# Performance work log

Measured on AMD Instinct MI355X. Metric: run time of the kernel, lower is better.

## Reference

```python
import jax, jax.numpy as jnp
import numpy as np

EPS = 1e-9
ALPHA = 1.0
BETA = 6.0
TOPK = 13
NUM_CLASSES = 80


def _make_boxes(key, shape, img=640.0, wh_min=8.0, wh_max=128.0):
    k1, k2 = jax.random.split(key)
    cxy = jax.random.uniform(k1, shape[:-1] + (2,)) * img
    wh = wh_min + jax.random.uniform(k2, shape[:-1] + (2,)) * (wh_max - wh_min)
    return jnp.concatenate([cxy - wh / 2, cxy + wh / 2], axis=-1)


def setup_inputs() -> dict:
    key = jax.random.key(0)
    ks = jax.random.split(key, 5)
    B, N, C, M = 16, 8400, NUM_CLASSES, 64
    pd_scores = jax.random.normal(ks[0], (B, N, C), dtype=jnp.float32)  # logits
    pd_bboxes = _make_boxes(ks[1], (B, N, 4))
    anc_points = jax.random.uniform(ks[2], (N, 2)) * 640.0
    gt_labels = jax.random.randint(ks[3], (B, M, 1), 0, C).astype(jnp.int64)
    gt_bboxes = _make_boxes(ks[4], (B, M, 4), wh_min=16.0, wh_max=256.0)
    mask_gt = jnp.ones((B, M, 1), dtype=jnp.float32)
    return {"pd_scores": pd_scores, "pd_bboxes": pd_bboxes, "anc_points": anc_points,
            "gt_labels": gt_labels, "gt_bboxes": gt_bboxes, "mask_gt": mask_gt}


def _pairwise_iou(gt_bboxes, pd_bboxes):
    # gt: (B,M,4), pd: (B,N,4) -> (B,M,N)
    a1 = gt_bboxes[:, :, None, :2]
    a2 = gt_bboxes[:, :, None, 2:]
    b1 = pd_bboxes[:, None, :, :2]
    b2 = pd_bboxes[:, None, :, 2:]
    inter = jnp.clip(jnp.minimum(a2, b2) - jnp.maximum(a1, b1), 0.0).prod(-1)
    area_a = (a2 - a1).prod(-1)
    area_b = (b2 - b1).prod(-1)
    return inter / jnp.maximum(area_a + area_b - inter, EPS)


def _tal_assign(pd_scores, pd_bboxes, anc_points, gt_labels, gt_bboxes, mask_gt):
    B, N, C = pd_scores.shape
    M = gt_labels.shape[1]
    ps = jax.nn.sigmoid(pd_scores)  # input_is_logits=True
    mask_gt_bool = mask_gt[..., 0] > 0.5  # (B,M)

    # centers-in-boxes mask (B,M,N)
    xy = anc_points[None, None, :, :]
    lt = gt_bboxes[:, :, None, :2]
    rb = gt_bboxes[:, :, None, 2:]
    deltas = jnp.concatenate([xy - lt, rb - xy], axis=-1)  # (B,M,N,4)
    mask_in_gts = deltas.min(-1) > EPS
    valid = mask_in_gts & mask_gt_bool[:, :, None]

    # alignment metric: score(gt class)^alpha * IoU^beta, zero outside valid
    gt_ids = jnp.clip(gt_labels[..., 0], 0)  # (B,M)
    scores_t = jnp.swapaxes(ps, 1, 2)  # (B,C,N)
    bbox_scores = jnp.take_along_axis(scores_t, gt_ids[:, :, None], axis=1)  # (B,M,N)
    ious = _pairwise_iou(gt_bboxes, pd_bboxes)
    ious = jnp.where(valid, ious, 0.0)
    align = jnp.where(valid, (bbox_scores ** ALPHA) * (ious ** BETA), 0.0)

    # top-k anchors per GT along anchor dim
    topv, topi = jax.lax.top_k(align, TOPK)  # (B,M,K)
    sel = (topv > EPS) & mask_gt_bool[:, :, None]
    bi = jnp.arange(B)[:, None, None]
    mi = jnp.arange(M)[None, :, None]
    cnt = jnp.zeros((B, M, N), jnp.int32).at[bi, mi, topi].add(sel.astype(jnp.int32))
    topk_mask = cnt > 0
    mask_pos = (topk_mask & valid).astype(jnp.float32)  # (B,M,N)

    # resolve anchors assigned to multiple GTs: keep highest IoU GT
    fg = mask_pos.sum(axis=1)  # (B,N)
    multi = (fg > 1)[:, None, :]  # (B,1,N)
    best_gt = jnp.argmax(ious, axis=1)  # (B,N)
    is_max = jnp.swapaxes(jax.nn.one_hot(best_gt, M, dtype=mask_pos.dtype), 1, 2)  # (B,M,N)
    mask_pos = jnp.where(multi, is_max, mask_pos)
    fg_mask = mask_pos.sum(axis=1)  # (B,N)
    tgt_gt_idx = jnp.argmax(mask_pos, axis=1)  # (B,N)

    # gather targets
    target_labels = jnp.take_along_axis(gt_labels[..., 0], tgt_gt_idx, axis=1)  # (B,N)
    target_bboxes = jnp.take_along_axis(gt_bboxes, tgt_gt_idx[..., None], axis=1)  # (B,N,4)

    # normalized classification targets
    align = align * mask_pos
    max_align = align.max(axis=1, keepdims=True) + EPS  # (B,1,N)
    per_anchor = (align / max_align * (ious * mask_pos)).sum(axis=1)  # (B,N)
    onehot = jax.nn.one_hot(target_labels, C, dtype=jnp.float32)
    cls_targets = onehot * per_anchor[..., None]  # (B,N,C)
    return target_labels, target_bboxes, cls_targets, fg_mask > 0, tgt_gt_idx


def reference(pd_scores, pd_bboxes, anc_points, gt_labels, gt_bboxes, mask_gt):
    return _tal_assign(pd_scores, pd_bboxes, anc_points, gt_labels, gt_bboxes, mask_gt)
```

## Files before the change

kernel.cpp:

```cpp
#include <hip/hip_runtime.h>
#include <math.h>

#define BB 16
#define NN 8400
#define CC 80
#define MM 64
#define KTOP 13
#define FEPS 1e-9f
#define CAP 2048
#define RPW 8

typedef float floatx4 __attribute__((ext_vector_type(4)));
typedef unsigned long long u64;

#define OFF_O1 134400
#define OFF_O2 672000
#define OFF_O3 11424000
#define OFF_O4 11558400
#define CCNT_OFF 6153472
#define CAND_OFF 6154496
#define SCR_OFF  10348800

__device__ __forceinline__ float iou_pair(const float4 g, const float4 p) {
    float ix1 = fmaxf(g.x, p.x);
    float iy1 = fmaxf(g.y, p.y);
    float ix2 = fminf(g.z, p.z);
    float iy2 = fminf(g.w, p.w);
    float iw = fmaxf(ix2 - ix1, 0.0f);
    float ih = fmaxf(iy2 - iy1, 0.0f);
    float inter = iw * ih;
    float aa = (g.z - g.x) * (g.w - g.y);
    float ab = (p.z - p.x) * (p.w - p.y);
    float uni = fmaxf(aa + ab - inter, FEPS);
    return inter / uni;
}

__global__ __launch_bounds__(256) void k_zero2(int* __restrict__ ccnt,
                                               int* __restrict__ scr)
{
    int i = blockIdx.x * 256 + threadIdx.x;
    if (i < 1024) ccnt[i] = 0;
    else if (i < 1024 + 403200) scr[i - 1024] = 0;
}

__global__ __launch_bounds__(256) void k_align_emit(
    const float* __restrict__ pd_scores, const float* __restrict__ pd_bboxes,
    const float* __restrict__ anc, const int* __restrict__ gt_labels,
    const float* __restrict__ gt_bboxes, const float* __restrict__ mask_gt,
    int* __restrict__ ccnt, u64* __restrict__ cand)
{
    const int b = blockIdx.y;
    const int n = blockIdx.x * 256 + threadIdx.x;
    const int tid = threadIdx.x;

    __shared__ float4 gtb[MM];
    __shared__ int labS[MM];
    __shared__ int hcnt[MM];
    __shared__ int gbase[MM];

    if (tid < MM) {
        float4 g = *(const float4*)&gt_bboxes[(size_t)(b * MM + tid) * 4];
        if (mask_gt[b * MM + tid] <= 0.5f)
            g = make_float4(1e30f, 1e30f, -1e30f, -1e30f);
        gtb[tid] = g;
        int lb = gt_labels[b * MM + tid];
        labS[tid] = lb > 0 ? lb : 0;
        hcnt[tid] = 0;
    }
    __syncthreads();

    float ax = 0.0f, ay = 0.0f;
    const bool inb = n < NN;
    if (inb) { float2 a2 = *(const float2*)&anc[2 * n]; ax = a2.x; ay = a2.y; }

    u64 mask = 0ull;
    #pragma unroll 8
    for (int m = 0; m < MM; ++m) {
        float4 g = gtb[m];
        float d1 = ax - g.x, d2 = ay - g.y, d3 = g.z - ax, d4 = g.w - ay;
        if (inb && fminf(fminf(d1, d2), fminf(d3, d4)) > FEPS)
            mask |= 1ull << m;
    }

    u64 t = mask;
    while (t) { int m = __ffsll(t) - 1; t &= t - 1; atomicAdd(&hcnt[m], 1); }
    __syncthreads();
    if (tid < MM && hcnt[tid] > 0) {
        gbase[tid] = atomicAdd(&ccnt[b * MM + tid], hcnt[tid]);
        hcnt[tid] = 0;
    }
    __syncthreads();

    if (mask) {
        const float4 p = *(const float4*)&pd_bboxes[((size_t)b * NN + n) * 4];
        const float* srow = pd_scores + ((size_t)b * NN + n) * CC;
        t = mask;
        while (t) {
            int m = __ffsll(t) - 1; t &= t - 1;
            float io = iou_pair(gtb[m], p);
            int lab = labS[m];
            float4 c = *(const float4*)(srow + (lab & ~3));
            int r = lab & 3;
            float x = (r == 0) ? c.x : (r == 1) ? c.y : (r == 2) ? c.z : c.w;
            float s = 1.0f / (1.0f + expf(-x));
            float i2 = io * io;
            unsigned key = __float_as_uint(s * (i2 * i2 * i2));
            int slot = gbase[m] + atomicAdd(&hcnt[m], 1);
            if (slot < CAP)
                cand[(size_t)(b * MM + m) * CAP + slot] =
                    ((u64)key << 32) | (unsigned)(NN - n);
        }
    }
}

__global__ __launch_bounds__(256) void k_topk(
    const int* __restrict__ ccnt, const u64* __restrict__ cand,
    int* __restrict__ cntb, int* __restrict__ mselb, float* __restrict__ aselb)
{
    const int bm = blockIdx.x;
    const int b = bm >> 6, m = bm & 63;
    const int tid = threadIdx.x;
    const int lane = tid & 63;
    const int wid = tid >> 6;

    __shared__ u64 cmerge[64];

    const unsigned epskey = __float_as_uint(FEPS);
    const int count = min(ccnt[bm], CAP);
    const u64* list = cand + (size_t)bm * CAP;

    u64 e[RPW];
    #pragma unroll
    for (int j = 0; j < RPW; ++j) {
        int i = tid + j * 256;
        e[j] = (i < count) ? list[i] : 0ull;
    }

    {
        u64 lm = 0ull;
        #pragma unroll
        for (int j = 0; j < RPW; ++j) if (e[j] > lm) lm = e[j];

        u64 winv = 0ull;
        for (int r = 0; r < KTOP; ++r) {
            u64 bv = lm;
            #pragma unroll
            for (int off = 32; off > 0; off >>= 1) {
                u64 ov = __shfl_xor(bv, off, 64);
                if (ov > bv) bv = ov;
            }
            if ((unsigned)(bv >> 32) <= epskey) break;
            if (lane == r) winv = bv;
            if (lm == bv) {
                #pragma unroll
                for (int j = 0; j < RPW; ++j) if (e[j] == bv) e[j] = 0ull;
                lm = 0ull;
                #pragma unroll
                for (int j = 0; j < RPW; ++j) if (e[j] > lm) lm = e[j];
            }
        }
        if (lane < KTOP) cmerge[wid * KTOP + lane] = winv;
        if (wid == 0 && lane >= 4 * KTOP) cmerge[lane] = 0ull;
    }
    __syncthreads();

    if (wid == 0) {
        u64 v = cmerge[lane];
        u64 winv = 0ull;
        for (int r = 0; r < KTOP; ++r) {
            u64 bv = v;
            #pragma unroll
            for (int off = 32; off > 0; off >>= 1) {
                u64 ov = __shfl_xor(bv, off, 64);
                if (ov > bv) bv = ov;
            }
            if ((unsigned)(bv >> 32) <= epskey) break;
            if (lane == r) winv = bv;
            if (v == bv) v = 0ull;
        }
        if (lane < KTOP) {
            unsigned hk = (unsigned)(winv >> 32);
            if (hk > epskey) {
                int n = NN - (int)(winv & 0xFFFFFFFFull);
                int ai = b * NN + n;
                atomicAdd(&cntb[ai], 1);
                atomicAdd(&mselb[ai], m);
                atomicAdd(&aselb[ai], __uint_as_float(hk));
            }
        }
    }
}

__global__ __launch_bounds__(256) void k_assign(
    const float* __restrict__ pd_scores, const float* __restrict__ pd_bboxes,
    const float* __restrict__ anc, const int* __restrict__ gt_labels,
    const float* __restrict__ gt_bboxes, const float* __restrict__ mask_gt,
    const int* __restrict__ cntb, const int* __restrict__ mselb,
    const float* __restrict__ aselb,
    float* __restrict__ out0, float* __restrict__ out1,
    float* __restrict__ out3, float* __restrict__ out4,
    float* __restrict__ perb)
{
    const int b = blockIdx.y;
    const int n = blockIdx.x * 256 + threadIdx.x;

    __shared__ float4 gtb[MM];
    __shared__ int    labS[MM];
    __shared__ float  mgS[MM];
    if (threadIdx.x < MM) {
        int m = threadIdx.x;
        gtb[m]  = *(const float4*)&gt_bboxes[(size_t)(b * MM + m) * 4];
        labS[m] = gt_labels[b * MM + m];
        mgS[m]  = mask_gt[b * MM + m];
    }
    __syncthreads();
    if (n >= NN) return;

    const size_t idx = (size_t)b * NN + n;
    const int cnt = cntb[idx];

    float per = 0.0f, fg = 0.0f;
    int mstar = 0;

    if (cnt > 0) {
        fg = 1.0f;
        const float4 p = *(const float4*)&pd_bboxes[idx * 4];
        if (cnt == 1) {
            mstar = mselb[idx];
            float a = aselb[idx];
            float io = iou_pair(gtb[mstar], p);
            per = a / (a + FEPS) * io;
        } else {
            float2 a2 = *(const float2*)&anc[2 * n];
            float bestI = -1.0f; int bestM = 0;
            for (int m = 0; m < MM; ++m) {
                float4 gg = gtb[m];
                float d1 = a2.x - gg.x, d2 = a2.y - gg.y;
                float d3 = gg.z - a2.x, d4 = gg.w - a2.y;
                bool valid = (fminf(fminf(d1, d2), fminf(d3, d4)) > FEPS) &&
                             (mgS[m] > 0.5f);
                float io = valid ? iou_pair(gg, p) : 0.0f;
                if (io > bestI) { bestI = io; bestM = m; }
            }
            mstar = bestM;
            float io = bestI;
            int lb = labS[mstar]; int lbc = lb > 0 ? lb : 0;
            float x = pd_scores[idx * CC + lbc];
            float s = 1.0f / (1.0f + expf(-x));
            float i2 = io * io;
            float a = s * (i2 * i2 * i2);
            per = a / (a + FEPS) * io;
        }
    }

    out0[idx] = (float)labS[mstar];
    ((float4*)out1)[idx] = gtb[mstar];
    out3[idx] = fg;
    out4[idx] = (float)mstar;
    perb[idx] = per;
}

__global__ __launch_bounds__(256) void k_cls(
    const float* __restrict__ out0, const float* __restrict__ perb,
    floatx4* __restrict__ cls4)
{
    int i = blockIdx.x * 256 + threadIdx.x;
    if (i >= BB * NN * CC / 4) return;
    int row = i / 20;
    int c4 = (i - row * 20) * 4;
    int lab = (int)out0[row];
    float per = perb[row];
    int d = lab - c4;
    floatx4 v;
    v.x = (d == 0) ? per : 0.0f;
    v.y = (d == 1) ? per : 0.0f;
    v.z = (d == 2) ? per : 0.0f;
    v.w = (d == 3) ? per : 0.0f;
    __builtin_nontemporal_store(v, &cls4[i]);
}

extern "C" void kernel_launch(void* const* d_in, const int* in_sizes, int n_in,
                              void* d_out, int out_size, void* d_ws, size_t ws_size,
                              hipStream_t stream) {
    const float* pd_scores = (const float*)d_in[0];
    const float* pd_bboxes = (const float*)d_in[1];
    const float* anc       = (const float*)d_in[2];
    const int*   gt_labels = (const int*)d_in[3];
    const float* gt_bboxes = (const float*)d_in[4];
    const float* mask_gt   = (const float*)d_in[5];

    float* out  = (float*)d_out;
    float* out0 = out;
    float* out1 = out + OFF_O1;
    float* out2 = out + OFF_O2;
    float* out3 = out + OFF_O3;
    float* out4 = out + OFF_O4;

    int*   ccnt  = (int*)(out2 + CCNT_OFF);
    u64*   cand  = (u64*)(out2 + CAND_OFF);
    float* scr   = out2 + SCR_OFF;
    int*   cntb  = (int*)scr;
    int*   mselb = (int*)(scr + 134400);
    float* aselb = scr + 268800;
    float* perb  = (float*)d_ws;

    k_zero2<<<dim3((1024 + 403200 + 255) / 256), dim3(256), 0, stream>>>(
        ccnt, (int*)scr);

    k_align_emit<<<dim3((NN + 255) / 256, BB), dim3(256), 0, stream>>>(
        pd_scores, pd_bboxes, anc, gt_labels, gt_bboxes, mask_gt, ccnt, cand);

    k_topk<<<dim3(BB * MM), dim3(256), 0, stream>>>(
        ccnt, cand, cntb, mselb, aselb);

    k_assign<<<dim3((NN + 255) / 256, BB), dim3(256), 0, stream>>>(
        pd_scores, pd_bboxes, anc, gt_labels, gt_bboxes, mask_gt,
        cntb, mselb, aselb, out0, out1, out3, out4, perb);

    const int n4 = (BB * NN * CC) / 4;
    k_cls<<<dim3((n4 + 255) / 256), dim3(256), 0, stream>>>(out0, perb, (floatx4*)out2);
}
```

Before: 64.15 us.

## Fuse assign with cls write, stage score rows in LDS, move scratch to workspace

The class-target write kernel is folded into the assign kernel, so each block writes its own one-hot rows from per-anchor label and score values kept in shared memory. This removes one launch and the perb round trip. The emit kernel now stages contiguous score rows and predicted boxes through shared memory in coalesced chunks, and spreads each anchor's GT candidates across 8 lanes instead of one thread doing scattered gathers. Scratch buffers move from the cls output region into the workspace, which keeps them from colliding with the fused cls writes. In exchange, the emit kernel reads every score row and adds extra barriers.

```diff
diff --git a/kernel.cpp b/kernel.cpp
--- a/kernel.cpp
+++ b/kernel.cpp
@@ -17,9 +17,8 @@
 #define OFF_O2 672000
 #define OFF_O3 11424000
 #define OFF_O4 11558400
-#define CCNT_OFF 6153472
-#define CAND_OFF 6154496
-#define SCR_OFF  10348800
+
+#define ZERO_N (1024 + 3 * 134400)
 
 __device__ __forceinline__ float iou_pair(const float4 g, const float4 p) {
     float ix1 = fmaxf(g.x, p.x);
@@ -35,12 +34,10 @@
     return inter / uni;
 }
 
-__global__ __launch_bounds__(256) void k_zero2(int* __restrict__ ccnt,
-                                               int* __restrict__ scr)
+__global__ __launch_bounds__(256) void k_zero(int* __restrict__ p)
 {
     int i = blockIdx.x * 256 + threadIdx.x;
-    if (i < 1024) ccnt[i] = 0;
-    else if (i < 1024 + 403200) scr[i - 1024] = 0;
+    if (i < ZERO_N) p[i] = 0;
 }
 
 __global__ __launch_bounds__(256) void k_align_emit(
@@ -50,13 +47,17 @@
     int* __restrict__ ccnt, u64* __restrict__ cand)
 {
     const int b = blockIdx.y;
-    const int n = blockIdx.x * 256 + threadIdx.x;
     const int tid = threadIdx.x;
+    const int n0 = blockIdx.x * 256;
+    const int n = n0 + tid;
 
     __shared__ float4 gtb[MM];
-    __shared__ int labS[MM];
-    __shared__ int hcnt[MM];
-    __shared__ int gbase[MM];
+    __shared__ int    labS[MM];
+    __shared__ int    hcnt[MM];
+    __shared__ int    gbase[MM];
+    __shared__ u64    maskS[256];
+    __shared__ float4 srows4[640];
+    __shared__ float4 pbbS[32];
 
     if (tid < MM) {
         float4 g = *(const float4*)&gt_bboxes[(size_t)(b * MM + tid) * 4];
@@ -81,6 +82,7 @@
         if (inb && fminf(fminf(d1, d2), fminf(d3, d4)) > FEPS)
             mask |= 1ull << m;
     }
+    maskS[tid] = mask;
 
     u64 t = mask;
     while (t) { int m = __ffsll(t) - 1; t &= t - 1; atomicAdd(&hcnt[m], 1); }
@@ -89,26 +91,48 @@
         gbase[tid] = atomicAdd(&ccnt[b * MM + tid], hcnt[tid]);
         hcnt[tid] = 0;
     }
-    __syncthreads();
-
-    if (mask) {
-        const float4 p = *(const float4*)&pd_bboxes[((size_t)b * NN + n) * 4];
-        const float* srow = pd_scores + ((size_t)b * NN + n) * CC;
-        t = mask;
-        while (t) {
-            int m = __ffsll(t) - 1; t &= t - 1;
-            float io = iou_pair(gtb[m], p);
-            int lab = labS[m];
-            float4 c = *(const float4*)(srow + (lab & ~3));
-            int r = lab & 3;
-            float x = (r == 0) ? c.x : (r == 1) ? c.y : (r == 2) ? c.z : c.w;
-            float s = 1.0f / (1.0f + expf(-x));
-            float i2 = io * io;
-            unsigned key = __float_as_uint(s * (i2 * i2 * i2));
-            int slot = gbase[m] + atomicAdd(&hcnt[m], 1);
-            if (slot < CAP)
-                cand[(size_t)(b * MM + m) * CAP + slot] =
-                    ((u64)key << 32) | (unsigned)(NN - n);
+
+    const float4* src4 = (const float4*)(pd_scores + (size_t)b * NN * CC);
+    for (int sub = 0; sub < 8; ++sub) {
+        const int la0 = sub * 32;
+        const int gn0 = n0 + la0;
+        __syncthreads();
+        {
+            const int base4 = gn0 * 20;
+            #pragma unroll
+            for (int k = tid; k < 640; k += 256) {
+                int gf = base4 + k;
+                srows4[k] = (gf < NN * 20) ? src4[gf]
+                                           : make_float4(0.f, 0.f, 0.f, 0.f);
+            }
+            if (tid < 32) {
+                int gn = gn0 + tid;
+                pbbS[tid] = (gn < NN)
+                    ? *(const float4*)&pd_bboxes[((size_t)b * NN + gn) * 4]
+                    : make_float4(0.f, 0.f, 0.f, 0.f);
+            }
+        }
+        __syncthreads();
+
+        const int la = la0 + (tid >> 3);
+        const int r = tid & 7;
+        u64 tt = maskS[la] & (0x0101010101010101ull << r);
+        if (tt) {
+            const float4 p = pbbS[la - la0];
+            const float* row = (const float*)srows4 + (la - la0) * 80;
+            const int gn = n0 + la;
+            while (tt) {
+                int m = __ffsll(tt) - 1; tt &= tt - 1;
+                float io = iou_pair(gtb[m], p);
+                float x = row[labS[m]];
+                float s = 1.0f / (1.0f + expf(-x));
+                float i2 = io * io;
+                unsigned key = __float_as_uint(s * (i2 * i2 * i2));
+                int slot = gbase[m] + atomicAdd(&hcnt[m], 1);
+                if (slot < CAP)
+                    cand[(size_t)(b * MM + m) * CAP + slot] =
+                        ((u64)key << 32) | (unsigned)(NN - gn);
+            }
         }
     }
 }
@@ -191,7 +215,7 @@
     }
 }
 
-__global__ __launch_bounds__(256) void k_assign(
+__global__ __launch_bounds__(256) void k_assign_cls(
     const float* __restrict__ pd_scores, const float* __restrict__ pd_bboxes,
     const float* __restrict__ anc, const int* __restrict__ gt_labels,
     const float* __restrict__ gt_bboxes, const float* __restrict__ mask_gt,
@@ -199,84 +223,88 @@
     const float* __restrict__ aselb,
     float* __restrict__ out0, float* __restrict__ out1,
     float* __restrict__ out3, float* __restrict__ out4,
-    float* __restrict__ perb)
+    floatx4* __restrict__ cls4)
 {
     const int b = blockIdx.y;
-    const int n = blockIdx.x * 256 + threadIdx.x;
+    const int n0 = blockIdx.x * 256;
+    const int tid = threadIdx.x;
+    const int n = n0 + tid;
 
     __shared__ float4 gtb[MM];
     __shared__ int    labS[MM];
     __shared__ float  mgS[MM];
-    if (threadIdx.x < MM) {
-        int m = threadIdx.x;
+    __shared__ int    labL[256];
+    __shared__ float  perL[256];
+
+    if (tid < MM) {
+        int m = tid;
         gtb[m]  = *(const float4*)&gt_bboxes[(size_t)(b * MM + m) * 4];
         labS[m] = gt_labels[b * MM + m];
         mgS[m]  = mask_gt[b * MM + m];
     }
     __syncthreads();
-    if (n >= NN) return;
-
-    const size_t idx = (size_t)b * NN + n;
-    const int cnt = cntb[idx];
 
     float per = 0.0f, fg = 0.0f;
     int mstar = 0;
 
-    if (cnt > 0) {
-        fg = 1.0f;
-        const float4 p = *(const float4*)&pd_bboxes[idx * 4];
-        if (cnt == 1) {
-            mstar = mselb[idx];
-            float a = aselb[idx];
-            float io = iou_pair(gtb[mstar], p);
-            per = a / (a + FEPS) * io;
-        } else {
-            float2 a2 = *(const float2*)&anc[2 * n];
-            float bestI = -1.0f; int bestM = 0;
-            for (int m = 0; m < MM; ++m) {
-                float4 gg = gtb[m];
-                float d1 = a2.x - gg.x, d2 = a2.y - gg.y;
-                float d3 = gg.z - a2.x, d4 = gg.w - a2.y;
-                bool valid = (fminf(fminf(d1, d2), fminf(d3, d4)) > FEPS) &&
-                             (mgS[m] > 0.5f);
-                float io = valid ? iou_pair(gg, p) : 0.0f;
-                if (io > bestI) { bestI = io; bestM = m; }
-            }
-            mstar = bestM;
-            float io = bestI;
-            int lb = labS[mstar]; int lbc = lb > 0 ? lb : 0;
-            float x = pd_scores[idx * CC + lbc];
-            float s = 1.0f / (1.0f + expf(-x));
-            float i2 = io * io;
-            float a = s * (i2 * i2 * i2);
-            per = a / (a + FEPS) * io;
-        }
-    }
-
-    out0[idx] = (float)labS[mstar];
-    ((float4*)out1)[idx] = gtb[mstar];
-    out3[idx] = fg;
-    out4[idx] = (float)mstar;
-    perb[idx] = per;
-}
-
-__global__ __launch_bounds__(256) void k_cls(
-    const float* __restrict__ out0, const float* __restrict__ perb,
-    floatx4* __restrict__ cls4)
-{
-    int i = blockIdx.x * 256 + threadIdx.x;
-    if (i >= BB * NN * CC / 4) return;
-    int row = i / 20;
-    int c4 = (i - row * 20) * 4;
-    int lab = (int)out0[row];
-    float per = perb[row];
-    int d = lab - c4;
-    floatx4 v;
-    v.x = (d == 0) ? per : 0.0f;
-    v.y = (d == 1) ? per : 0.0f;
-    v.z = (d == 2) ? per : 0.0f;
-    v.w = (d == 3) ? per : 0.0f;
-    __builtin_nontemporal_store(v, &cls4[i]);
+    if (n < NN) {
+        const size_t idx = (size_t)b * NN + n;
+        const int cnt = cntb[idx];
+        if (cnt > 0) {
+            fg = 1.0f;
+            const float4 p = *(const float4*)&pd_bboxes[idx * 4];
+            if (cnt == 1) {
+                mstar = mselb[idx];
+                float a = aselb[idx];
+                float io = iou_pair(gtb[mstar], p);
+                per = a / (a + FEPS) * io;
+            } else {
+                float2 a2 = *(const float2*)&anc[2 * n];
+                float bestI = -1.0f; int bestM = 0;
+                for (int m = 0; m < MM; ++m) {
+                    float4 gg = gtb[m];
+                    float d1 = a2.x - gg.x, d2 = a2.y - gg.y;
+                    float d3 = gg.z - a2.x, d4 = gg.w - a2.y;
+                    bool valid = (fminf(fminf(d1, d2), fminf(d3, d4)) > FEPS) &&
+                                 (mgS[m] > 0.5f);
+                    float io = valid ? iou_pair(gg, p) : 0.0f;
+                    if (io > bestI) { bestI = io; bestM = m; }
+                }
+                mstar = bestM;
+                float io = bestI;
+                int lb = labS[mstar]; int lbc = lb > 0 ? lb : 0;
+                float x = pd_scores[idx * CC + lbc];
+                float s = 1.0f / (1.0f + expf(-x));
+                float i2 = io * io;
+                float a = s * (i2 * i2 * i2);
+                per = a / (a + FEPS) * io;
+            }
+        }
+        out0[idx] = (float)labS[mstar];
+        ((float4*)out1)[idx] = gtb[mstar];
+        out3[idx] = fg;
+        out4[idx] = (float)mstar;
+    }
+    labL[tid] = (n < NN) ? labS[mstar] : 0;
+    perL[tid] = per;
+    __syncthreads();
+
+    const size_t base4 = ((size_t)b * NN + n0) * 20;
+    for (int k = tid; k < 5120; k += 256) {
+        int lrow = k / 20;
+        int gn = n0 + lrow;
+        if (gn >= NN) break;
+        int c4 = (k - lrow * 20) * 4;
+        int lab = labL[lrow];
+        float pr = perL[lrow];
+        int d = lab - c4;
+        floatx4 v;
+        v.x = (d == 0) ? pr : 0.0f;
+        v.y = (d == 1) ? pr : 0.0f;
+        v.z = (d == 2) ? pr : 0.0f;
+        v.w = (d == 3) ? pr : 0.0f;
+        __builtin_nontemporal_store(v, &cls4[base4 + k]);
+    }
 }
 
 extern "C" void kernel_launch(void* const* d_in, const int* in_sizes, int n_in,
@@ -296,16 +324,14 @@
     float* out3 = out + OFF_O3;
     float* out4 = out + OFF_O4;
 
-    int*   ccnt  = (int*)(out2 + CCNT_OFF);
-    u64*   cand  = (u64*)(out2 + CAND_OFF);
-    float* scr   = out2 + SCR_OFF;
-    int*   cntb  = (int*)scr;
-    int*   mselb = (int*)(scr + 134400);
-    float* aselb = scr + 268800;
-    float* perb  = (float*)d_ws;
-
-    k_zero2<<<dim3((1024 + 403200 + 255) / 256), dim3(256), 0, stream>>>(
-        ccnt, (int*)scr);
+    int*   ws_i  = (int*)d_ws;
+    int*   ccnt  = ws_i;
+    int*   cntb  = ws_i + 1024;
+    int*   mselb = ws_i + 1024 + 134400;
+    float* aselb = (float*)(ws_i + 1024 + 2 * 134400);
+    u64*   cand  = (u64*)((char*)d_ws + (size_t)ZERO_N * 4);
+
+    k_zero<<<dim3((ZERO_N + 255) / 256), dim3(256), 0, stream>>>(ws_i);
 
     k_align_emit<<<dim3((NN + 255) / 256, BB), dim3(256), 0, stream>>>(
         pd_scores, pd_bboxes, anc, gt_labels, gt_bboxes, mask_gt, ccnt, cand);
@@ -313,10 +339,7 @@
     k_topk<<<dim3(BB * MM), dim3(256), 0, stream>>>(
         ccnt, cand, cntb, mselb, aselb);
 
-    k_assign<<<dim3((NN + 255) / 256, BB), dim3(256), 0, stream>>>(
+    k_assign_cls<<<dim3((NN + 255) / 256, BB), dim3(256), 0, stream>>>(
         pd_scores, pd_bboxes, anc, gt_labels, gt_bboxes, mask_gt,
-        cntb, mselb, aselb, out0, out1, out3, out4, perb);
-
-    const int n4 = (BB * NN * CC) / 4;
-    k_cls<<<dim3((n4 + 255) / 256), dim3(256), 0, stream>>>(out0, perb, (floatx4*)out2);
-}
+        cntb, mselb, aselb, out0, out1, out3, out4, (floatx4*)out2);
+}
```

Result: slower. 71.05 us (+10.8%).
